# Performance work log

Hardware: AMD Instinct MI355X
Metric: run time of the kernel (lower is better)

The kernel has to match this reference:

```python
import jax, jax.numpy as jnp
import numpy as np

B = 8
GXN, GYN = 240, 121  # internal lon/lat grid sizes


def nearest_resize(x, oh, ow):
    # torch F.interpolate mode='nearest' on NCHW: idx = floor(i * in/out)
    H, W = x.shape[2], x.shape[3]
    hi = (jnp.arange(oh) * H) // oh
    wi = (jnp.arange(ow) * W) // ow
    return x[:, :, hi][:, :, :, wi]


def _kern(p, g, ls):
    # p: (B,N), g: (G,) -> (B,N,G) RBF weights
    d = p[:, :, None] - g[None, None, :]
    return jnp.exp(-0.5 * d * d / (ls * ls))


def setconv_off_to_on(px, py, y, gx, gy, ls, eps=1e-6):
    # Off-grid points -> grid. px,py: (B,N); y: (B,C,N).
    fin = jnp.isfinite(y)
    m = fin.astype(y.dtype)
    yv = jnp.where(fin, y, 0.0)
    kx = _kern(px, gx, ls)  # (B,N,Gx)
    ky = _kern(py, gy, ls)  # (B,N,Gy)

    def per_ch(args):
        mc, yc = args  # (B,N) each
        den = jnp.einsum('bni,bnj->bij', kx * mc[:, :, None], ky)
        sig = jnp.einsum('bni,bnj->bij', kx * yc[:, :, None], ky)
        return den, sig

    den, sig = jax.lax.map(per_ch, (jnp.swapaxes(m, 0, 1), jnp.swapaxes(yv, 0, 1)))
    den = jnp.swapaxes(den, 0, 1)  # (B,C,Gx,Gy)
    sig = jnp.swapaxes(sig, 0, 1) / (den + eps)
    Bb, C = y.shape[0], y.shape[1]
    return jnp.stack([den, sig], axis=2).reshape(Bb, 2 * C, gx.shape[0], gy.shape[0])


def setconv_on_to_on(xlon, xlat, w, gx, gy, ls, eps=1e-6):
    # Source grid -> internal grid, separable RBF. xlon:(B,H), xlat:(B,W), w:(B,C,H,W).
    fin = jnp.isfinite(w)
    m = fin.astype(w.dtype)
    wv = jnp.where(fin, w, 0.0)
    kx = _kern(xlon, gx, ls)  # (B,H,Gx)
    ky = _kern(xlat, gy, ls)  # (B,W,Gy)
    den = jnp.einsum('bchw,bhi,bwj->bcij', m, kx, ky)
    sig = jnp.einsum('bchw,bhi,bwj->bcij', wv, kx, ky) / (den + eps)
    Bb, C = w.shape[0], w.shape[1]
    return jnp.stack([den, sig], axis=2).reshape(Bb, 2 * C, gx.shape[0], gy.shape[0])


def _forward(iasi_current, ascat_current, hadisd_x, hadisd_y, icoads_x, icoads_current, sat_x_lon, sat_x_lat, sat_current, amsua_x_lon, amsua_x_lat, amsua_current, amsub_x_lon, amsub_x_lat, amsub_current, hirs_x_lon, hirs_x_lat, hirs_current, igra_x, igra_current, era5_elev, climatology, aux_time, ls):
    lsv = ls[0]
    gx = (jnp.linspace(0.0, 360.0, GXN) / 360.0).astype(jnp.float32)
    gy = (jnp.linspace(-90.0, 90.0, GYN) / 360.0).astype(jnp.float32)
    enc = []
    # IASI / ASCAT: nan->0, nearest interp to (240,121), flip lat axis
    e = nearest_resize(jnp.transpose(jnp.nan_to_num(iasi_current), (0, 3, 1, 2)), GXN, GYN)
    enc.append(jnp.flip(e, axis=-1))
    e = nearest_resize(jnp.transpose(jnp.nan_to_num(ascat_current), (0, 3, 1, 2)), GXN, GYN)
    enc.append(jnp.flip(e, axis=-1))
    # HadISD: 4 off-grid channels
    had = [setconv_off_to_on(hadisd_x[c, :, 0], hadisd_x[c, :, 1], hadisd_y[c][:, None, :], gx, gy, lsv) for c in range(4)]
    enc.append(jnp.concatenate(had, axis=1))
    # ICOADS: 5 off-grid channels (shared point cloud)
    enc.append(setconv_off_to_on(icoads_x[:, 0], icoads_x[:, 1], icoads_current, gx, gy, lsv))
    # GRIDSAT: 2 on-grid channels
    enc.append(setconv_on_to_on(sat_x_lon, sat_x_lat, sat_current, gx, gy, lsv))
    # AMSU-A: last channel nan'd, zeros nan'd, permute(0,3,2,1)
    w = jnp.transpose(amsua_current, (0, 3, 2, 1))  # (B,13,240,121)
    w = w.at[:, -1].set(jnp.nan)
    w = jnp.where(w == 0.0, jnp.nan, w)
    enc.append(setconv_on_to_on(amsua_x_lon, amsua_x_lat, w, gx, gy, lsv))
    # AMSU-B: zeros nan'd, permute(0,3,1,2)
    w = jnp.transpose(amsub_current, (0, 3, 1, 2))
    w = jnp.where(w == 0.0, jnp.nan, w)
    enc.append(setconv_on_to_on(amsub_x_lon, amsub_x_lat, w, gx, gy, lsv))
    # IGRA: 24 off-grid channels
    enc.append(setconv_off_to_on(igra_x[:, 0], igra_x[:, 1], igra_current, gx, gy, lsv))
    # HIRS: 26 on-grid channels
    w = jnp.transpose(hirs_current, (0, 3, 1, 2))
    w = jnp.where(w == 0.0, jnp.nan, w)
    enc.append(setconv_on_to_on(hirs_x_lon, hirs_x_lat, w, gx, gy, lsv))
    # Elevation: permute, flip, nearest interp to internal grid
    el = jnp.flip(jnp.transpose(era5_elev, (0, 1, 3, 2)), axis=2)
    el = nearest_resize(el, GYN, GXN)  # (B,1,121,240)
    enc.append(jnp.transpose(el, (0, 1, 3, 2)))  # align to (B,1,240,121)
    enc.append(climatology)
    enc.append(jnp.ones_like(climatology[:, :1]) * aux_time[:, :, None, None])
    x = jnp.concatenate(enc, axis=1)  # (B,213,240,121)
    return x


def setup_inputs() -> dict:
    key = jax.random.key(0)
    ks = jax.random.split(key, 24)
    f32 = jnp.float32
    d = {}
    d['iasi_current'] = jax.random.normal(ks[0], (B, 120, 60, 8), f32)
    d['ascat_current'] = jax.random.normal(ks[1], (B, 120, 60, 3), f32)
    hx = jax.random.uniform(ks[2], (4, B, 2, 5000), f32)
    d['hadisd_x'] = hx.at[:, :, 1].set(hx[:, :, 1] * 0.5 - 0.25)
    d['hadisd_y'] = jax.random.normal(ks[3], (4, B, 5000), f32)
    ix = jax.random.uniform(ks[4], (B, 2, 20000), f32)
    d['icoads_x'] = ix.at[:, 1].set(ix[:, 1] * 0.5 - 0.25)
    d['icoads_current'] = jax.random.normal(ks[5], (B, 5, 20000), f32)
    d['sat_x_lon'] = jnp.sort(jax.random.uniform(ks[6], (B, 360), f32), axis=-1)
    d['sat_x_lat'] = jnp.sort(jax.random.uniform(ks[7], (B, 180), f32) * 0.5 - 0.25, axis=-1)
    d['sat_current'] = jax.random.normal(ks[8], (B, 2, 360, 180), f32)
    d['amsua_x_lon'] = jnp.sort(jax.random.uniform(ks[9], (B, 240), f32), axis=-1)
    d['amsua_x_lat'] = jnp.sort(jax.random.uniform(ks[10], (B, 121), f32) * 0.5 - 0.25, axis=-1)
    d['amsua_current'] = jax.random.normal(ks[11], (B, 121, 240, 13), f32)
    d['amsub_x_lon'] = jnp.sort(jax.random.uniform(ks[12], (B, 240), f32), axis=-1)
    d['amsub_x_lat'] = jnp.sort(jax.random.uniform(ks[13], (B, 121), f32) * 0.5 - 0.25, axis=-1)
    d['amsub_current'] = jax.random.normal(ks[14], (B, 240, 121, 12), f32)
    d['hirs_x_lon'] = jnp.sort(jax.random.uniform(ks[15], (B, 240), f32), axis=-1)
    d['hirs_x_lat'] = jnp.sort(jax.random.uniform(ks[16], (B, 121), f32) * 0.5 - 0.25, axis=-1)
    d['hirs_current'] = jax.random.normal(ks[17], (B, 240, 121, 26), f32)
    gxp = jax.random.uniform(ks[18], (B, 2, 3000), f32)
    d['igra_x'] = gxp.at[:, 1].set(gxp[:, 1] * 0.5 - 0.25)
    d['igra_current'] = jax.random.normal(ks[19], (B, 24, 3000), f32)
    d['era5_elev'] = jax.random.normal(ks[20], (B, 1, 480, 242), f32)
    d['climatology'] = jax.random.normal(ks[21], (B, 24, 240, 121), f32)
    d['aux_time'] = jax.random.normal(ks[22], (B, 5), f32)
    d['ls'] = jnp.full((1,), 0.001, f32)  # learned RBF lengthscale (init 0.001)
    return d


def reference(iasi_current, ascat_current, hadisd_x, hadisd_y, icoads_x, icoads_current, sat_x_lon, sat_x_lat, sat_current, amsua_x_lon, amsua_x_lat, amsua_current, amsub_x_lon, amsub_x_lat, amsub_current, hirs_x_lon, hirs_x_lat, hirs_current, igra_x, igra_current, era5_elev, climatology, aux_time, ls):
    return _forward(iasi_current, ascat_current, hadisd_x, hadisd_y, icoads_x, icoads_current, sat_x_lon, sat_x_lat, sat_current, amsua_x_lon, amsua_x_lat, amsua_current, amsub_x_lon, amsub_x_lat, amsub_current, hirs_x_lon, hirs_x_lat, hirs_current, igra_x, igra_current, era5_elev, climatology, aux_time, ls)
```

## Files before the change

kernel.cpp:

```cpp
#include <hip/hip_runtime.h>
#include <cmath>

#define GXN 240
#define GYN 121
#define SP  29040
#define NB  8
#define NCH 213
#define EPSV 1e-6f
#define DMAXF 7.75f
#define ACLIP -30.0f

#define P_HAD   160000
#define P_ICO   160000
#define P_IGRA  24000
#define PT_TOT  344000
#define VB_TOT  48
#define NCELL   (VB_TOT*SP)

__device__ __forceinline__ float gxv(int i){ return (float)i * (1.0f/239.0f); }
__device__ __forceinline__ float gyv(int j){ return -0.25f + (float)j * (1.0f/240.0f); }
__device__ __forceinline__ size_t oidx(int b,int c,int i,int j){
  return (((size_t)b*NCH + c)*GXN + i)*GYN + j;
}
__device__ __forceinline__ int binx(float x){
  int i = (int)floorf(x*239.0f + 0.5f);
  return i<0?0:(i>239?239:i);
}
__device__ __forceinline__ int biny(float y){
  int j = (int)floorf((y+0.25f)*240.0f + 0.5f);
  return j<0?0:(j>120?120:j);
}
__device__ __forceinline__ int lbnd(const float* a, int n, float v){
  int lo=0, hi=n;
  while(lo<hi){ int m=(lo+hi)>>1; if(a[m]<v) lo=m+1; else hi=m; }
  return lo;
}
__device__ __forceinline__ int ubnd(const float* a, int n, float v){
  int lo=0, hi=n;
  while(lo<hi){ int m=(lo+hi)>>1; if(a[m]<=v) lo=m+1; else hi=m; }
  return lo;
}

struct PtLoc { int ds, vb, n; float x, y; };
__device__ __forceinline__ PtLoc ptloc(int idx, const float* hadx, const float* icx, const float* igx){
  PtLoc p;
  if(idx < P_HAD){
    p.ds=0; p.vb=idx/5000; p.n=idx%5000;
    p.x = hadx[(size_t)p.vb*10000 + p.n];
    p.y = hadx[(size_t)p.vb*10000 + 5000 + p.n];
  } else if(idx < P_HAD + P_ICO){
    int t = idx - P_HAD; p.ds=1; p.vb=t/20000; p.n=t%20000;
    p.x = icx[(size_t)p.vb*40000 + p.n];
    p.y = icx[(size_t)p.vb*40000 + 20000 + p.n];
  } else {
    int t = idx - (P_HAD+P_ICO); p.ds=2; p.vb=t/3000; p.n=t%3000;
    p.x = igx[(size_t)p.vb*6000 + p.n];
    p.y = igx[(size_t)p.vb*6000 + 3000 + p.n];
  }
  return p;
}
__device__ __forceinline__ int vbglobal(const PtLoc& p){
  return (p.ds==0)? p.vb : (p.ds==1? 32+p.vb : 40+p.vb);
}

__global__ void kzero_i(int* __restrict__ p, int n){
  int i = blockIdx.x*blockDim.x + threadIdx.x;
  if(i<n) p[i]=0;
}

__global__ void kcount(const float* __restrict__ hadx, const float* __restrict__ icx,
                       const float* __restrict__ igx, int* __restrict__ counts){
  int idx = blockIdx.x*blockDim.x + threadIdx.x;
  if(idx >= PT_TOT) return;
  PtLoc p = ptloc(idx, hadx, icx, igx);
  atomicAdd(counts + vbglobal(p)*SP + binx(p.x)*GYN + biny(p.y), 1);
}

__global__ void kscan1(const int* __restrict__ in, int* __restrict__ part,
                       int* __restrict__ bsum, int n){
  __shared__ int ts[256];
  int t = threadIdx.x;
  int base = blockIdx.x*1024 + t*4;
  int v0=0,v1=0,v2=0,v3=0;
  if(base+0<n) v0=in[base+0];
  if(base+1<n) v1=in[base+1];
  if(base+2<n) v2=in[base+2];
  if(base+3<n) v3=in[base+3];
  ts[t]=v0+v1+v2+v3; __syncthreads();
  for(int off=1; off<256; off<<=1){
    int x = (t>=off)? ts[t-off] : 0; __syncthreads();
    ts[t]+=x; __syncthreads();
  }
  int ex = (t==0)? 0 : ts[t-1];
  if(base+0<n) part[base+0]=ex;
  if(base+1<n) part[base+1]=ex+v0;
  if(base+2<n) part[base+2]=ex+v0+v1;
  if(base+3<n) part[base+3]=ex+v0+v1+v2;
  if(t==255) bsum[blockIdx.x]=ts[255];
}

__global__ void kscan2(int* __restrict__ b, int n){
  __shared__ int ts[256];
  int t = threadIdx.x;
  int v[16]; int s=0;
#pragma unroll
  for(int k=0;k<16;k++){ int p=t*16+k; v[k] = (p<n)? b[p] : 0; s+=v[k]; }
  ts[t]=s; __syncthreads();
  for(int off=1; off<256; off<<=1){
    int x = (t>=off)? ts[t-off] : 0; __syncthreads();
    ts[t]+=x; __syncthreads();
  }
  int run = (t==0)? 0 : ts[t-1];
#pragma unroll
  for(int k=0;k<16;k++){ int p=t*16+k; if(p<n) b[p]=run; run+=v[k]; }
}

__global__ void kscan3(const int* __restrict__ part, const int* __restrict__ bsum,
                       int* __restrict__ offs, int* __restrict__ cursor, int n){
  int i = blockIdx.x*blockDim.x + threadIdx.x;
  if(i==0) offs[n] = PT_TOT;
  if(i>=n) return;
  int v = part[i] + bsum[i>>10];
  offs[i]=v; cursor[i]=v;
}

__global__ void kpack(const float* __restrict__ hadx, const float* __restrict__ icx,
                      const float* __restrict__ igx,
                      const float* __restrict__ hady, const float* __restrict__ icy,
                      const float* __restrict__ igy,
                      int* __restrict__ cursor,
                      float* __restrict__ had_rec, float* __restrict__ ico_rec,
                      float* __restrict__ igra_rec){
  int idx = blockIdx.x*blockDim.x + threadIdx.x;
  if(idx >= PT_TOT) return;
  PtLoc p = ptloc(idx, hadx, icx, igx);
  int cell = vbglobal(p)*SP + binx(p.x)*GYN + biny(p.y);
  int pos = atomicAdd(cursor + cell, 1);
  if(p.ds==0){
    float* r = had_rec + (size_t)pos*4;
    r[0]=p.x; r[1]=p.y;
    r[2]=hady[(size_t)p.vb*5000 + p.n];
  } else if(p.ds==1){
    float* r = ico_rec + (size_t)(pos - P_HAD)*8;
    r[0]=p.x; r[1]=p.y;
#pragma unroll
    for(int c=0;c<5;c++) r[2+c]=icy[((size_t)p.vb*5 + c)*20000 + p.n];
  } else {
    float* r = igra_rec + (size_t)(pos - P_HAD - P_ICO)*28;
    r[0]=p.x; r[1]=p.y;
#pragma unroll
    for(int c=0;c<24;c++) r[2+c]=igy[((size_t)p.vb*24 + c)*3000 + p.n];
  }
}

template<int C, int RS>
__global__ void kgoff(const float* __restrict__ rec, const int* __restrict__ offs,
                      int vbBase, int dsBase, int nvb, int chBase,
                      const float* __restrict__ lsp, float* __restrict__ out){
  int idx = blockIdx.x*blockDim.x + threadIdx.x;
  if(idx >= nvb*SP) return;
  int vb = idx/SP; int cell = idx%SP; int i = cell/GYN; int j = cell%GYN;
  int b = vb & 7; int set = vb >> 3;
  int vbG = vbBase + vb;
  float ls = lsp[0];
  float inv2 = 0.5f/(ls*ls);
  float dmax = DMAXF*ls;
  int rbx = (int)floorf(dmax*239.0f + 0.5f);
  int rby = (int)floorf(dmax*240.0f + 0.5f);
  float gi = gxv(i), gj = gyv(j);
  float den[C], sig[C];
#pragma unroll
  for(int c=0;c<C;c++){ den[c]=0.f; sig[c]=0.f; }
  int ilo = i-rbx; if(ilo<0) ilo=0;
  int ihi = i+rbx; if(ihi>GXN-1) ihi=GXN-1;
  int jlo = j-rby; if(jlo<0) jlo=0;
  int jhi = j+rby; if(jhi>GYN-1) jhi=GYN-1;
  int jspan = jhi - jlo;
  for(int bi=ilo; bi<=ihi; bi++){
    int cb0 = vbG*SP + bi*GYN + jlo;
    int s = offs[cb0] - dsBase;
    int e = offs[cb0 + jspan + 1] - dsBase;
    for(int t=s; t<e; t++){
      const float* r = rec + (size_t)t*RS;
      float dx = r[0]-gi, dy = r[1]-gj;
      float a = -(dx*dx + dy*dy)*inv2;
      if(a < ACLIP) continue;
      float wt = expf(a);
#pragma unroll
      for(int c=0;c<C;c++){
        float v = r[2+c];
        if(isfinite(v)){ den[c]+=wt; sig[c]+=wt*v; }
      }
    }
  }
#pragma unroll
  for(int c=0;c<C;c++){
    size_t d = oidx(b, chBase + set*2*C + 2*c, i, j);
    out[d]    = den[c];
    out[d+SP] = sig[c]/(den[c]+EPSV);
  }
}

__global__ void kcopy(const float* __restrict__ iasi, const float* __restrict__ ascat,
                      const float* __restrict__ elev, const float* __restrict__ clim,
                      const float* __restrict__ aux, float* __restrict__ out){
  int idx = blockIdx.x*blockDim.x + threadIdx.x;
  if(idx >= NB*41*SP) return;
  int j = idx%GYN; int i=(idx/GYN)%GXN; int cc=(idx/SP)%41; int b=idx/(SP*41);
  float v; int oc;
  if(cc < 8){
    int hi = i>>1, wi = ((120 - j)*60)/121;
    v = iasi[((b*120 + hi)*60 + wi)*8 + cc];
    if(!isfinite(v)) v = isnan(v) ? 0.f : (v>0.f? 3.4028235e38f : -3.4028235e38f);
    oc = cc;
  } else if(cc < 11){
    int hi = i>>1, wi = ((120 - j)*60)/121;
    v = ascat[((b*120 + hi)*60 + wi)*3 + (cc-8)];
    if(!isfinite(v)) v = isnan(v) ? 0.f : (v>0.f? 3.4028235e38f : -3.4028235e38f);
    oc = cc;
  } else if(cc == 11){
    v = elev[(b*480 + 2*i)*242 + (241 - 2*j)];
    oc = 183;
  } else if(cc < 36){
    int c = cc-12;
    v = clim[(((size_t)b*24 + c)*GXN + i)*GYN + j];
    oc = 184 + c;
  } else {
    v = aux[b*5 + (cc-36)];
    oc = 208 + (cc-36);
  }
  out[oidx(b,oc,i,j)] = v;
}

template<int C, int MODE>
__global__ void kon(const float* __restrict__ xlon, const float* __restrict__ xlat,
                    const float* __restrict__ src, int H, int W, int chBase,
                    const float* __restrict__ lsp, float* __restrict__ out){
  int idx = blockIdx.x*blockDim.x + threadIdx.x;
  if(idx >= NB*SP) return;
  int j=idx%GYN; int i=(idx/GYN)%GXN; int b=idx/SP;
  float ls = lsp[0];
  float inv2 = 0.5f/(ls*ls);
  float dmax = DMAXF*ls;
  float gi = gxv(i), gj = gyv(j);
  const float* lon = xlon + b*H;
  const float* lat = xlat + b*W;
  int hlo = lbnd(lon,H,gi-dmax), hhi = ubnd(lon,H,gi+dmax);
  int wlo = lbnd(lat,W,gj-dmax), whi = ubnd(lat,W,gj+dmax);
  float den[C], sig[C];
#pragma unroll
  for(int c=0;c<C;c++){ den[c]=0.f; sig[c]=0.f; }
  for(int h=hlo; h<hhi; h++){
    float dx = lon[h]-gi;
    float ax = -dx*dx*inv2;
    if(ax < ACLIP) continue;
    for(int w=wlo; w<whi; w++){
      float dy = lat[w]-gj;
      float a = ax - dy*dy*inv2;
      if(a < ACLIP) continue;
      float wt = expf(a);
      const float* s;
      if(MODE==0)      s = src + ((size_t)b*C*H + h)*W + w;
      else if(MODE==1) s = src + (((size_t)b*W + w)*H + h)*C;
      else             s = src + (((size_t)b*H + h)*W + w)*C;
#pragma unroll
      for(int c=0;c<C;c++){
        float v = (MODE==0) ? s[(size_t)c*H*W] : s[c];
        bool ok = isfinite(v);
        if(MODE>=1) ok = ok && (v!=0.0f);
        if(MODE==1 && c==C-1) ok = false;
        if(ok){ den[c]+=wt; sig[c]+=wt*v; }
      }
    }
  }
#pragma unroll
  for(int c=0;c<C;c++){
    size_t d = oidx(b,chBase+2*c,i,j);
    out[d]    = den[c];
    out[d+SP] = sig[c]/(den[c]+EPSV);
  }
}

extern "C" void kernel_launch(void* const* d_in, const int* in_sizes, int n_in,
                              void* d_out, int out_size, void* d_ws, size_t ws_size,
                              hipStream_t stream){
  const float* iasi  = (const float*)d_in[0];
  const float* ascat = (const float*)d_in[1];
  const float* hadx  = (const float*)d_in[2];
  const float* hady  = (const float*)d_in[3];
  const float* icx   = (const float*)d_in[4];
  const float* icy   = (const float*)d_in[5];
  const float* slon  = (const float*)d_in[6];
  const float* slat  = (const float*)d_in[7];
  const float* scur  = (const float*)d_in[8];
  const float* alon  = (const float*)d_in[9];
  const float* alat  = (const float*)d_in[10];
  const float* acur  = (const float*)d_in[11];
  const float* blon  = (const float*)d_in[12];
  const float* blat  = (const float*)d_in[13];
  const float* bcur  = (const float*)d_in[14];
  const float* hlon  = (const float*)d_in[15];
  const float* hlat  = (const float*)d_in[16];
  const float* hcur  = (const float*)d_in[17];
  const float* igx   = (const float*)d_in[18];
  const float* igy   = (const float*)d_in[19];
  const float* elev  = (const float*)d_in[20];
  const float* clim  = (const float*)d_in[21];
  const float* aux   = (const float*)d_in[22];
  const float* ls    = (const float*)d_in[23];
  float* out = (float*)d_out;
  dim3 tb(256);
  auto nb = [](long long n){ return dim3((unsigned)((n+255)/256)); };

  int* counts = (int*)d_ws;
  int* offs   = counts + NCELL;
  int* bsum   = offs + NCELL + 1;
  float* had_rec  = (float*)(bsum + 4096);
  float* ico_rec  = had_rec + 640000;
  float* igra_rec = ico_rec + 1280000;

  int nblk = (NCELL + 1023)/1024;

  kcopy<<<nb((long long)NB*41*SP),tb,0,stream>>>(iasi, ascat, elev, clim, aux, out);

  kzero_i<<<nb(NCELL),tb,0,stream>>>(counts, NCELL);
  kcount <<<nb(PT_TOT),tb,0,stream>>>(hadx, icx, igx, counts);
  kscan1 <<<dim3(nblk),tb,0,stream>>>(counts, offs, bsum, NCELL);
  kscan2 <<<dim3(1),tb,0,stream>>>(bsum, nblk);
  kscan3 <<<nb(NCELL),tb,0,stream>>>(offs, bsum, offs, counts, NCELL);
  kpack  <<<nb(PT_TOT),tb,0,stream>>>(hadx, icx, igx, hady, icy, igy,
                                      counts, had_rec, ico_rec, igra_rec);

  kgoff<1,4>  <<<nb((long long)32*SP),tb,0,stream>>>(had_rec,  offs,  0, 0,               32, 11, ls, out);
  kgoff<5,8>  <<<nb((long long)NB*SP),tb,0,stream>>>(ico_rec,  offs, 32, P_HAD,            8, 19, ls, out);
  kgoff<24,28><<<nb((long long)NB*SP),tb,0,stream>>>(igra_rec, offs, 40, P_HAD+P_ICO,      8, 83, ls, out);

  kon<2,0> <<<nb((long long)NB*SP),tb,0,stream>>>(slon, slat, scur, 360, 180, 29, ls, out);
  kon<13,1><<<nb((long long)NB*SP),tb,0,stream>>>(alon, alat, acur, 240, 121, 33, ls, out);
  kon<12,2><<<nb((long long)NB*SP),tb,0,stream>>>(blon, blat, bcur, 240, 121, 59, ls, out);
  kon<26,2><<<nb((long long)NB*SP),tb,0,stream>>>(hlon, hlat, hcur, 240, 121, 131, ls, out);
}
```

Baseline: 747.8 us.

## Fuse copy, on-grid and off-grid setconv kernels into one channel-grouped megakernel

```diff
diff --git a/kernel.cpp b/kernel.cpp
--- a/kernel.cpp
+++ b/kernel.cpp
@@ -16,6 +16,8 @@
 #define PT_TOT  344000
 #define VB_TOT  48
 #define NCELL   (VB_TOT*SP)
+#define CBLK    908
+#define NGROUP  39
 
 __device__ __forceinline__ float gxv(int i){ return (float)i * (1.0f/239.0f); }
 __device__ __forceinline__ float gyv(int j){ return -0.25f + (float)j * (1.0f/240.0f); }
@@ -153,60 +155,10 @@
   }
 }
 
-template<int C, int RS>
-__global__ void kgoff(const float* __restrict__ rec, const int* __restrict__ offs,
-                      int vbBase, int dsBase, int nvb, int chBase,
-                      const float* __restrict__ lsp, float* __restrict__ out){
-  int idx = blockIdx.x*blockDim.x + threadIdx.x;
-  if(idx >= nvb*SP) return;
-  int vb = idx/SP; int cell = idx%SP; int i = cell/GYN; int j = cell%GYN;
-  int b = vb & 7; int set = vb >> 3;
-  int vbG = vbBase + vb;
-  float ls = lsp[0];
-  float inv2 = 0.5f/(ls*ls);
-  float dmax = DMAXF*ls;
-  int rbx = (int)floorf(dmax*239.0f + 0.5f);
-  int rby = (int)floorf(dmax*240.0f + 0.5f);
-  float gi = gxv(i), gj = gyv(j);
-  float den[C], sig[C];
-#pragma unroll
-  for(int c=0;c<C;c++){ den[c]=0.f; sig[c]=0.f; }
-  int ilo = i-rbx; if(ilo<0) ilo=0;
-  int ihi = i+rbx; if(ihi>GXN-1) ihi=GXN-1;
-  int jlo = j-rby; if(jlo<0) jlo=0;
-  int jhi = j+rby; if(jhi>GYN-1) jhi=GYN-1;
-  int jspan = jhi - jlo;
-  for(int bi=ilo; bi<=ihi; bi++){
-    int cb0 = vbG*SP + bi*GYN + jlo;
-    int s = offs[cb0] - dsBase;
-    int e = offs[cb0 + jspan + 1] - dsBase;
-    for(int t=s; t<e; t++){
-      const float* r = rec + (size_t)t*RS;
-      float dx = r[0]-gi, dy = r[1]-gj;
-      float a = -(dx*dx + dy*dy)*inv2;
-      if(a < ACLIP) continue;
-      float wt = expf(a);
-#pragma unroll
-      for(int c=0;c<C;c++){
-        float v = r[2+c];
-        if(isfinite(v)){ den[c]+=wt; sig[c]+=wt*v; }
-      }
-    }
-  }
-#pragma unroll
-  for(int c=0;c<C;c++){
-    size_t d = oidx(b, chBase + set*2*C + 2*c, i, j);
-    out[d]    = den[c];
-    out[d+SP] = sig[c]/(den[c]+EPSV);
-  }
-}
-
-__global__ void kcopy(const float* __restrict__ iasi, const float* __restrict__ ascat,
-                      const float* __restrict__ elev, const float* __restrict__ clim,
-                      const float* __restrict__ aux, float* __restrict__ out){
-  int idx = blockIdx.x*blockDim.x + threadIdx.x;
-  if(idx >= NB*41*SP) return;
-  int j = idx%GYN; int i=(idx/GYN)%GXN; int cc=(idx/SP)%41; int b=idx/(SP*41);
+__device__ __forceinline__ void copy_one(int cc, int b, int i, int j,
+    const float* __restrict__ iasi, const float* __restrict__ ascat,
+    const float* __restrict__ elev, const float* __restrict__ clim,
+    const float* __restrict__ aux, float* __restrict__ out){
   float v; int oc;
   if(cc < 8){
     int hi = i>>1, wi = ((120 - j)*60)/121;
@@ -232,52 +184,149 @@
   out[oidx(b,oc,i,j)] = v;
 }
 
-template<int C, int MODE>
-__global__ void kon(const float* __restrict__ xlon, const float* __restrict__ xlat,
-                    const float* __restrict__ src, int H, int W, int chBase,
-                    const float* __restrict__ lsp, float* __restrict__ out){
-  int idx = blockIdx.x*blockDim.x + threadIdx.x;
-  if(idx >= NB*SP) return;
-  int j=idx%GYN; int i=(idx/GYN)%GXN; int b=idx/SP;
-  float ls = lsp[0];
-  float inv2 = 0.5f/(ls*ls);
-  float dmax = DMAXF*ls;
+__device__ __forceinline__ void ongrid(const float* __restrict__ lon, const float* __restrict__ lat,
+    const float* __restrict__ base, int H, int W, int sH, int sW, int sC,
+    int c0, int cg, int maskedC, bool zmask, int chOut,
+    float inv2, float dmax, int b, int i, int j, float* __restrict__ out){
   float gi = gxv(i), gj = gyv(j);
-  const float* lon = xlon + b*H;
-  const float* lat = xlat + b*W;
   int hlo = lbnd(lon,H,gi-dmax), hhi = ubnd(lon,H,gi+dmax);
   int wlo = lbnd(lat,W,gj-dmax), whi = ubnd(lat,W,gj+dmax);
-  float den[C], sig[C];
-#pragma unroll
-  for(int c=0;c<C;c++){ den[c]=0.f; sig[c]=0.f; }
+  float den[4]={0.f,0.f,0.f,0.f}, sig[4]={0.f,0.f,0.f,0.f};
   for(int h=hlo; h<hhi; h++){
     float dx = lon[h]-gi;
     float ax = -dx*dx*inv2;
     if(ax < ACLIP) continue;
+    const float* rowp = base + (size_t)h*sH + (size_t)c0*sC;
     for(int w=wlo; w<whi; w++){
       float dy = lat[w]-gj;
       float a = ax - dy*dy*inv2;
       if(a < ACLIP) continue;
       float wt = expf(a);
-      const float* s;
-      if(MODE==0)      s = src + ((size_t)b*C*H + h)*W + w;
-      else if(MODE==1) s = src + (((size_t)b*W + w)*H + h)*C;
-      else             s = src + (((size_t)b*H + h)*W + w)*C;
-#pragma unroll
-      for(int c=0;c<C;c++){
-        float v = (MODE==0) ? s[(size_t)c*H*W] : s[c];
-        bool ok = isfinite(v);
-        if(MODE>=1) ok = ok && (v!=0.0f);
-        if(MODE==1 && c==C-1) ok = false;
-        if(ok){ den[c]+=wt; sig[c]+=wt*v; }
+      const float* s = rowp + (size_t)w*sW;
+#pragma unroll
+      for(int c=0;c<4;c++){
+        if(c<cg){
+          float v = s[c*sC];
+          bool ok = isfinite(v);
+          if(zmask) ok = ok && (v!=0.0f);
+          if(c0+c == maskedC) ok = false;
+          if(ok){ den[c]+=wt; sig[c]+=wt*v; }
+        }
       }
     }
   }
 #pragma unroll
-  for(int c=0;c<C;c++){
-    size_t d = oidx(b,chBase+2*c,i,j);
-    out[d]    = den[c];
-    out[d+SP] = sig[c]/(den[c]+EPSV);
+  for(int c=0;c<4;c++){
+    if(c<cg){
+      size_t d = oidx(b, chOut + 2*c, i, j);
+      out[d]    = den[c];
+      out[d+SP] = sig[c]/(den[c]+EPSV);
+    }
+  }
+}
+
+__device__ __forceinline__ void offgrid(const float* __restrict__ rec, int RS,
+    const int* __restrict__ offs, int dsBase, int vbG, int voff, int cg, int chOut,
+    float inv2, float dmax, int b, int i, int j, float* __restrict__ out){
+  int rbx = (int)floorf(dmax*239.0f + 0.5f);
+  int rby = (int)floorf(dmax*240.0f + 0.5f);
+  float gi = gxv(i), gj = gyv(j);
+  int ilo = i-rbx; if(ilo<0) ilo=0;
+  int ihi = i+rbx; if(ihi>GXN-1) ihi=GXN-1;
+  int jlo = j-rby; if(jlo<0) jlo=0;
+  int jhi = j+rby; if(jhi>GYN-1) jhi=GYN-1;
+  int jspan = jhi - jlo;
+  float den[4]={0.f,0.f,0.f,0.f}, sig[4]={0.f,0.f,0.f,0.f};
+  for(int bi=ilo; bi<=ihi; bi++){
+    int cb0 = vbG*SP + bi*GYN + jlo;
+    int s = offs[cb0] - dsBase;
+    int e = offs[cb0 + jspan + 1] - dsBase;
+    for(int t=s; t<e; t++){
+      const float* r = rec + (size_t)t*RS;
+      float dx = r[0]-gi, dy = r[1]-gj;
+      float a = -(dx*dx + dy*dy)*inv2;
+      if(a < ACLIP) continue;
+      float wt = expf(a);
+#pragma unroll
+      for(int c=0;c<4;c++){
+        if(c<cg){
+          float v = r[voff+c];
+          if(isfinite(v)){ den[c]+=wt; sig[c]+=wt*v; }
+        }
+      }
+    }
+  }
+#pragma unroll
+  for(int c=0;c<4;c++){
+    if(c<cg){
+      size_t d = oidx(b, chOut + 2*c, i, j);
+      out[d]    = den[c];
+      out[d+SP] = sig[c]/(den[c]+EPSV);
+    }
+  }
+}
+
+__global__ __launch_bounds__(256) void kmega(
+    const float* __restrict__ iasi, const float* __restrict__ ascat,
+    const float* __restrict__ elev, const float* __restrict__ clim,
+    const float* __restrict__ aux,
+    const float* __restrict__ slon, const float* __restrict__ slat, const float* __restrict__ scur,
+    const float* __restrict__ alon, const float* __restrict__ alat, const float* __restrict__ acur,
+    const float* __restrict__ blon, const float* __restrict__ blat, const float* __restrict__ bcur,
+    const float* __restrict__ hlon, const float* __restrict__ hlat, const float* __restrict__ hcur,
+    const float* __restrict__ had_rec, const float* __restrict__ ico_rec,
+    const float* __restrict__ igra_rec, const int* __restrict__ offs,
+    const float* __restrict__ lsp, float* __restrict__ out){
+  int g = blockIdx.x / CBLK;
+  int t = (blockIdx.x % CBLK)*blockDim.x + threadIdx.x;
+  if(t >= NB*SP) return;
+  int j = t%GYN; int i = (t/GYN)%GXN; int b = t/SP;
+  float ls = lsp[0];
+  float inv2 = 0.5f/(ls*ls);
+  float dmax = DMAXF*ls;
+
+  if(g < 11){
+    int cb = g*4;
+#pragma unroll
+    for(int k=0;k<4;k++){
+      int cc = cb+k;
+      if(cc < 41) copy_one(cc, b, i, j, iasi, ascat, elev, clim, aux, out);
+    }
+  } else if(g < 13){
+    int c0 = g-11;
+    ongrid(slon + b*360, slat + b*180, scur + (size_t)b*2*360*180,
+           360, 180, 180, 1, 64800, c0, 1, -1, false, 29 + 2*c0,
+           inv2, dmax, b, i, j, out);
+  } else if(g < 17){
+    int c0 = (g-13)*4;
+    int cg = 13-c0 < 4 ? 13-c0 : 4;
+    ongrid(alon + b*240, alat + b*121, acur + (size_t)b*121*240*13,
+           240, 121, 13, 3120, 1, c0, cg, 12, true, 33 + 2*c0,
+           inv2, dmax, b, i, j, out);
+  } else if(g < 20){
+    int c0 = (g-17)*4;
+    ongrid(blon + b*240, blat + b*121, bcur + (size_t)b*240*121*12,
+           240, 121, 1452, 12, 1, c0, 4, -1, true, 59 + 2*c0,
+           inv2, dmax, b, i, j, out);
+  } else if(g < 27){
+    int c0 = (g-20)*4;
+    int cg = 26-c0 < 4 ? 26-c0 : 4;
+    ongrid(hlon + b*240, hlat + b*121, hcur + (size_t)b*240*121*26,
+           240, 121, 3146, 26, 1, c0, cg, -1, true, 131 + 2*c0,
+           inv2, dmax, b, i, j, out);
+  } else if(g < 31){
+    int set = g-27;
+    offgrid(had_rec, 4, offs, 0, set*8 + b, 2, 1, 11 + 2*set,
+            inv2, dmax, b, i, j, out);
+  } else if(g < 33){
+    int c0 = (g-31)*4;
+    int cg = 5-c0 < 4 ? 5-c0 : 4;
+    offgrid(ico_rec, 8, offs, P_HAD, 32 + b, 2 + c0, cg, 19 + 2*c0,
+            inv2, dmax, b, i, j, out);
+  } else {
+    int c0 = (g-33)*4;
+    offgrid(igra_rec, 28, offs, P_HAD + P_ICO, 40 + b, 2 + c0, 4, 83 + 2*c0,
+            inv2, dmax, b, i, j, out);
   }
 }
 
@@ -321,8 +370,6 @@
 
   int nblk = (NCELL + 1023)/1024;
 
-  kcopy<<<nb((long long)NB*41*SP),tb,0,stream>>>(iasi, ascat, elev, clim, aux, out);
-
   kzero_i<<<nb(NCELL),tb,0,stream>>>(counts, NCELL);
   kcount <<<nb(PT_TOT),tb,0,stream>>>(hadx, icx, igx, counts);
   kscan1 <<<dim3(nblk),tb,0,stream>>>(counts, offs, bsum, NCELL);
@@ -331,12 +378,7 @@
   kpack  <<<nb(PT_TOT),tb,0,stream>>>(hadx, icx, igx, hady, icy, igy,
                                       counts, had_rec, ico_rec, igra_rec);
 
-  kgoff<1,4>  <<<nb((long long)32*SP),tb,0,stream>>>(had_rec,  offs,  0, 0,               32, 11, ls, out);
-  kgoff<5,8>  <<<nb((long long)NB*SP),tb,0,stream>>>(ico_rec,  offs, 32, P_HAD,            8, 19, ls, out);
-  kgoff<24,28><<<nb((long long)NB*SP),tb,0,stream>>>(igra_rec, offs, 40, P_HAD+P_ICO,      8, 83, ls, out);
-
-  kon<2,0> <<<nb((long long)NB*SP),tb,0,stream>>>(slon, slat, scur, 360, 180, 29, ls, out);
-  kon<13,1><<<nb((long long)NB*SP),tb,0,stream>>>(alon, alat, acur, 240, 121, 33, ls, out);
-  kon<12,2><<<nb((long long)NB*SP),tb,0,stream>>>(blon, blat, bcur, 240, 121, 59, ls, out);
-  kon<26,2><<<nb((long long)NB*SP),tb,0,stream>>>(hlon, hlat, hcur, 240, 121, 131, ls, out);
-}
+  kmega<<<dim3(NGROUP*CBLK),tb,0,stream>>>(iasi, ascat, elev, clim, aux,
+      slon, slat, scur, alon, alat, acur, blon, blat, bcur, hlon, hlat, hcur,
+      had_rec, ico_rec, igra_rec, offs, ls, out);
+}
```

Measured after the change: 805.1 us. +7.7%, slower.
